# Optimization experiments

Hardware: AMD Instinct MI355X
Metric: run time of the kernel (lower is better)

Reference implementation:

```python
import jax, jax.numpy as jnp
import numpy as np
import math

B, N, D = 8, 4096, 1024
H = 8          # num_heads
NC = 2         # n_classes


def setup_inputs() -> dict:
    key = jax.random.key(0)
    ks = jax.random.split(key, 12)
    s = 1.0 / math.sqrt(D)
    return {
        "inputs": jax.random.normal(ks[0], (B, N, D), jnp.float32),
        # enc: Linear(D, 1) + Sigmoid
        "W_enc": jax.random.normal(ks[1], (1, D), jnp.float32) * s,
        "b_enc": jnp.zeros((1,), jnp.float32),
        "cls_token": jax.random.normal(ks[2], (1, 1, D), jnp.float32) * s,
        # depthwise Conv2d(D, D, 3, padding=1, groups=D)
        "conv_w": jax.random.normal(ks[3], (D, 1, 3, 3), jnp.float32) * 0.1,
        "conv_b": jnp.zeros((D,), jnp.float32),
        # MAB projections (torch Linear weight layout [out, in])
        "Wq": jax.random.normal(ks[4], (D, D), jnp.float32) * s,
        "bq": jnp.zeros((D,), jnp.float32),
        "Wk": jax.random.normal(ks[5], (D, D), jnp.float32) * s,
        "bk": jnp.zeros((D,), jnp.float32),
        "Wv": jax.random.normal(ks[6], (D, D), jnp.float32) * s,
        "bv": jnp.zeros((D,), jnp.float32),
        "Wo": jax.random.normal(ks[7], (D, D), jnp.float32) * s,
        "bo": jnp.zeros((D,), jnp.float32),
        # final classifier Linear(D, NC)
        "Wfc": jax.random.normal(ks[8], (NC, D), jnp.float32) * s,
        "bfc": jnp.zeros((NC,), jnp.float32),
    }


def reference(inputs, W_enc, b_enc, cls_token, conv_w, conv_b,
              Wq, bq, Wk, bk, Wv, bv, Wo, bo, Wfc, bfc):
    b, n, d = inputs.shape
    # ---- recalib(option='max', k=1): top-1 instance per bag as query ----
    a1 = jax.nn.sigmoid(inputs @ W_enc.T + b_enc)[..., 0]            # [B, N]
    idx = jnp.argmax(a1, axis=1)                                      # [B]
    Q = jnp.take_along_axis(inputs, idx[:, None, None], axis=1)       # [B, 1, D]
    # ---- shift_feature ----
    inputs = jax.nn.relu(inputs - Q)
    # ---- pad to square grid, prepend cls token ----
    _H = int(np.ceil(np.sqrt(n)))
    add = _H * _H - n
    x = jnp.concatenate([inputs, inputs[:, :add, :]], axis=1)         # [B, _H*_H, D]
    cls = jnp.broadcast_to(cls_token, (b, 1, d))
    x = jnp.concatenate([cls, x], axis=1)                             # [B, S, D]
    cls_tok, feat = x[:, 0], x[:, 1:]
    # ---- depthwise conv residual on the 2D grid ----
    cnn = feat.transpose(0, 2, 1).reshape(b, d, _H, _H)               # [B, C, H, W]
    conv = jax.lax.conv_general_dilated(
        cnn, conv_w, window_strides=(1, 1), padding='SAME',
        dimension_numbers=('NCHW', 'OIHW', 'NCHW'),
        feature_group_count=d) + conv_b[None, :, None, None]
    cnn = conv + cnn
    xf = cnn.reshape(b, d, _H * _H).transpose(0, 2, 1)
    x = jnp.concatenate([cls_tok[:, None, :], xf], axis=1)            # [B, S, D]
    # ---- MAB(Q, x): manual multi-head attention ----
    Qp = Q @ Wq.T + bq                                                # [B, 1, D]
    K = x @ Wk.T + bk                                                 # [B, S, D]
    V = x @ Wv.T + bv
    dh = d // H
    qh = Qp.reshape(b, 1, H, dh).transpose(0, 2, 1, 3)                # [B, H, 1, dh]
    kh = K.reshape(b, -1, H, dh).transpose(0, 2, 1, 3)                # [B, H, S, dh]
    vh = V.reshape(b, -1, H, dh).transpose(0, 2, 1, 3)
    # NOTE: original scales by sqrt(dim_V), not sqrt(d_head)
    logits = jnp.einsum('bhqd,bhkd->bhqk', qh, kh) / jnp.asarray(math.sqrt(d), jnp.float32)
    A = jax.nn.softmax(logits, axis=-1)
    oh = qh + jnp.einsum('bhqk,bhkd->bhqd', A, vh)                    # residual inside heads
    O = oh.transpose(0, 2, 1, 3).reshape(b, 1, d)                     # [B, 1, D]
    O = O + jax.nn.relu(O @ Wo.T + bo)
    bag = O[:, 0]                                                     # [B, D]
    out = bag @ Wfc.T + bfc                                           # [B, NC]
    return out
```

## Files before the change

### kernel.cpp

```cpp
#include <hip/hip_runtime.h>
#include <hip/hip_bf16.h>


#define NTOK 4096
#define DD 1024

#define FO_ARG 0
#define FO_S1  16
#define FO_CWT 4160
#define FO_QP  13376
#define FO_W   21568
#define FO_MS  87232
#define FO_YP  95424
#define FO_Y   4289728
#define FO_O1  4355264
#define FO_O2  4363456
#define FO_AW  4371648

#define LSTRIDE 101

__global__ void k_init(const float* __restrict__ convw, float* __restrict__ cwT) {
  int gid = blockIdx.x * 256 + threadIdx.x;
  if (gid < 9216) {
    int d = gid / 9, p = gid - d * 9;
    cwT[p * DD + d] = convw[gid];
  }
}

__global__ void k_argmax1(const float* __restrict__ inp, const float* __restrict__ Wenc,
                          const float* __restrict__ benc, unsigned long long* __restrict__ s1buf) {
  __shared__ unsigned long long lb[4];
  int wave = threadIdx.x >> 6, lane = threadIdx.x & 63;
  int b = blockIdx.x >> 8;
  int r0 = ((blockIdx.x & 255) << 4) + (wave << 2);
  const float4* base = (const float4*)(inp + ((size_t)b * NTOK + r0) * DD);
  const float4* wp = (const float4*)Wenc;
  float s0 = 0.f, s1 = 0.f, s2 = 0.f, s3 = 0.f;
#pragma unroll
  for (int k = 0; k < 4; ++k) {
    int off = lane + (k << 6);
    float4 w4 = wp[off];
    float4 a0 = base[off];
    float4 a1 = base[256 + off];
    float4 a2 = base[512 + off];
    float4 a3 = base[768 + off];
    s0 = fmaf(w4.x, a0.x, s0); s0 = fmaf(w4.y, a0.y, s0); s0 = fmaf(w4.z, a0.z, s0); s0 = fmaf(w4.w, a0.w, s0);
    s1 = fmaf(w4.x, a1.x, s1); s1 = fmaf(w4.y, a1.y, s1); s1 = fmaf(w4.z, a1.z, s1); s1 = fmaf(w4.w, a1.w, s1);
    s2 = fmaf(w4.x, a2.x, s2); s2 = fmaf(w4.y, a2.y, s2); s2 = fmaf(w4.z, a2.z, s2); s2 = fmaf(w4.w, a2.w, s2);
    s3 = fmaf(w4.x, a3.x, s3); s3 = fmaf(w4.y, a3.y, s3); s3 = fmaf(w4.z, a3.z, s3); s3 = fmaf(w4.w, a3.w, s3);
  }
#pragma unroll
  for (int mk = 32; mk >= 1; mk >>= 1) {
    s0 += __shfl_xor(s0, mk); s1 += __shfl_xor(s1, mk);
    s2 += __shfl_xor(s2, mk); s3 += __shfl_xor(s3, mk);
  }
  if (lane == 0) {
    float be = benc[0];
    float v[4] = {s0 + be, s1 + be, s2 + be, s3 + be};
    unsigned long long bst = 0ull;
#pragma unroll
    for (int i = 0; i < 4; ++i) {
      unsigned u = __float_as_uint(v[i]);
      u = (u & 0x80000000u) ? ~u : (u | 0x80000000u);
      unsigned long long p = ((unsigned long long)u << 32) |
                             (unsigned long long)(0xFFFFFFFFu - (unsigned)(r0 + i));
      bst = bst > p ? bst : p;
    }
    lb[wave] = bst;
  }
  __syncthreads();
  if (threadIdx.x == 0) {
    unsigned long long m = lb[0];
#pragma unroll
    for (int i = 1; i < 4; ++i) m = m > lb[i] ? m : lb[i];
    s1buf[blockIdx.x] = m;
  }
}

__global__ void k_argmax2(const unsigned long long* __restrict__ s1buf,
                          unsigned long long* __restrict__ argbest) {
  __shared__ unsigned long long red[256];
  int tid = threadIdx.x, b = blockIdx.x;
  red[tid] = s1buf[b * 256 + tid];
  __syncthreads();
  for (int s = 128; s > 0; s >>= 1) {
    if (tid < s) { unsigned long long o = red[tid + s]; if (o > red[tid]) red[tid] = o; }
    __syncthreads();
  }
  if (tid == 0) argbest[b] = red[0];
}

__global__ void k_qp(const float* __restrict__ inp, const float* __restrict__ Wq,
                     const float* __restrict__ bq, const unsigned long long* __restrict__ argbest,
                     float* __restrict__ Qp) {
  int wave = threadIdx.x >> 6, lane = threadIdx.x & 63;
  int b = blockIdx.x >> 8;
  int i = ((blockIdx.x & 255) << 2) + wave;
  unsigned idx = 0xFFFFFFFFu - (unsigned)(argbest[b] & 0xFFFFFFFFull);
  const float4* qr = (const float4*)(inp + ((size_t)b * NTOK + idx) * DD);
  const float4* wr = (const float4*)(Wq + (size_t)i * DD);
  float s = 0.f;
#pragma unroll
  for (int k = 0; k < 4; ++k) {
    float4 a = wr[lane + (k << 6)], x = qr[lane + (k << 6)];
    s = fmaf(a.x, x.x, s); s = fmaf(a.y, x.y, s);
    s = fmaf(a.z, x.z, s); s = fmaf(a.w, x.w, s);
  }
  for (int m = 32; m > 0; m >>= 1) s += __shfl_xor(s, m);
  if (lane == 0) Qp[b * DD + i] = s + bq[i];
}

__global__ void k_w(const float* __restrict__ Wk, const float* __restrict__ Qp,
                    float* __restrict__ wbuf) {
  __shared__ float qs[1024];
  __shared__ float sred[2048];
  const int tid = threadIdx.x;
  const int h = blockIdx.x >> 5, jb = blockIdx.x & 31;
  {
    int b = tid >> 5, i4 = tid & 31;
    ((float4*)qs)[b * 32 + i4] = ((const float4*)Qp)[b * 256 + (h << 5) + i4];
  }
  __syncthreads();
  const int jl = tid & 31, ig = tid >> 5;
  const float* wkp = Wk + (size_t)((h << 7) + (ig << 4)) * DD + (jb << 5) + jl;
  float acc[8];
#pragma unroll
  for (int b = 0; b < 8; ++b) acc[b] = 0.f;
#pragma unroll
  for (int ii = 0; ii < 16; ++ii) {
    float wv = wkp[(size_t)ii * DD];
    int i = (ig << 4) + ii;
#pragma unroll
    for (int b = 0; b < 8; ++b) acc[b] = fmaf(qs[(b << 7) + i], wv, acc[b]);
  }
#pragma unroll
  for (int b = 0; b < 8; ++b) sred[ig * 256 + (b << 5) + jl] = acc[b];
  __syncthreads();
  {
    int b = tid >> 5, j2 = tid & 31;
    float s = 0.f;
#pragma unroll
    for (int g = 0; g < 8; ++g) s += sred[g * 256 + (b << 5) + j2];
    wbuf[(size_t)((b << 3) + h) * DD + (jb << 5) + j2] = s;
  }
}

__global__ __launch_bounds__(512, 4) void k_logits(
    const float* __restrict__ inp, const float* __restrict__ convb,
    const float* __restrict__ cwT, const float* __restrict__ wbuf,
    const unsigned long long* __restrict__ argbest,
    float* __restrict__ plog) {
  __shared__ float4 sred4[32 * LSTRIDE];
  const int tid = threadIdx.x, bx = blockIdx.x;
  const int b = bx >> 9, tile = (bx >> 3) & 63, cidx = bx & 7;
  const int R0 = (tile >> 3) << 3, C0 = (tile & 7) << 3;
  const unsigned idxq = 0xFFFFFFFFu - (unsigned)(argbest[b] & 0xFFFFFFFFull);
  const float* inpb = inp + (size_t)b * NTOK * DD;
  const float* qrow = inpb + (size_t)idxq * DD;
  const int gg = tid & 31, ts = tid >> 5;
  const int jg = tid >> 5, rq = (tid >> 3) & 3, ca = tid & 7;
  const int r0a = rq << 1;
  const int jc = cidx << 7;

  float acc[2][8];
#pragma unroll
  for (int i = 0; i < 2; ++i)
#pragma unroll
    for (int h = 0; h < 8; ++h) acc[i][h] = 0.f;

  {
    const int js = jc + (gg << 2);
    float4 qv = *(const float4*)(qrow + js);
    for (int t = ts; t < 100; t += 16) {
      int tr = t / 10, tc = t - tr * 10;
      int gr = R0 - 1 + tr, gc = C0 - 1 + tc;
      float4 v = make_float4(0.f, 0.f, 0.f, 0.f);
      if (gr >= 0 && gr < 64 && gc >= 0 && gc < 64) {
        float4 rv = *(const float4*)(inpb + (size_t)((gr << 6) + gc) * DD + js);
        v.x = fmaxf(rv.x - qv.x, 0.f); v.y = fmaxf(rv.y - qv.y, 0.f);
        v.z = fmaxf(rv.z - qv.z, 0.f); v.w = fmaxf(rv.w - qv.w, 0.f);
      }
      sred4[gg * LSTRIDE + t] = v;
    }
  }
  __syncthreads();
#pragma unroll
  for (int sub = 0; sub < 2; ++sub) {
    const int g = (sub << 4) + jg;
    const int j4 = jc + (g << 2);
    float4 cwr[9];
#pragma unroll
    for (int p = 0; p < 9; ++p) cwr[p] = *(const float4*)(cwT + p * DD + j4);
    float4 cb4 = *(const float4*)(convb + j4);
    const float4* fb = sred4 + g * LSTRIDE;
    float4 x0 = cb4, x1 = cb4;
    {
      float4 rw[4][3];
#pragma unroll
      for (int rr = 0; rr < 4; ++rr)
#pragma unroll
        for (int dc = 0; dc < 3; ++dc)
          rw[rr][dc] = fb[(r0a + rr) * 10 + ca + dc];
#pragma unroll
      for (int dr = 0; dr < 3; ++dr)
#pragma unroll
        for (int dc = 0; dc < 3; ++dc) {
          float4 w = cwr[dr * 3 + dc];
          float4 f0 = rw[dr][dc], f1 = rw[dr + 1][dc];
          x0.x = fmaf(w.x, f0.x, x0.x); x0.y = fmaf(w.y, f0.y, x0.y);
          x0.z = fmaf(w.z, f0.z, x0.z); x0.w = fmaf(w.w, f0.w, x0.w);
          x1.x = fmaf(w.x, f1.x, x1.x); x1.y = fmaf(w.y, f1.y, x1.y);
          x1.z = fmaf(w.z, f1.z, x1.z); x1.w = fmaf(w.w, f1.w, x1.w);
        }
      x0.x += rw[1][1].x; x0.y += rw[1][1].y; x0.z += rw[1][1].z; x0.w += rw[1][1].w;
      x1.x += rw[2][1].x; x1.y += rw[2][1].y; x1.z += rw[2][1].z; x1.w += rw[2][1].w;
    }
#pragma unroll
    for (int h = 0; h < 8; ++h) {
      float4 whv = *(const float4*)(wbuf + (size_t)(b * 8 + h) * DD + j4);
      float a0 = acc[0][h], a1 = acc[1][h];
      a0 = fmaf(whv.x, x0.x, a0); a0 = fmaf(whv.y, x0.y, a0);
      a0 = fmaf(whv.z, x0.z, a0); a0 = fmaf(whv.w, x0.w, a0);
      a1 = fmaf(whv.x, x1.x, a1); a1 = fmaf(whv.y, x1.y, a1);
      a1 = fmaf(whv.z, x1.z, a1); a1 = fmaf(whv.w, x1.w, a1);
      acc[0][h] = a0; acc[1][h] = a1;
    }
  }
  __syncthreads();
  float* red = (float*)sred4;
#pragma unroll
  for (int it = 0; it < 2; ++it)
#pragma unroll
    for (int h = 0; h < 8; ++h)
      red[jg * 512 + ((r0a + it) * 8 + ca) * 8 + h] = acc[it][h];
  __syncthreads();
  {
    float s = 0.f;
#pragma unroll
    for (int g = 0; g < 16; ++g) s += red[g * 512 + tid];
    plog[(size_t)bx * 512 + tid] = s;
  }
}

__global__ void k_sm(const float* __restrict__ plog, float* __restrict__ aw,
                     float2* __restrict__ msbuf) {
  __shared__ float atile[512];
  const int tid = threadIdx.x, bt = blockIdx.x;
  const float* pp = plog + (size_t)bt * 8 * 512;
  float s0 = 0.f, s1 = 0.f;
#pragma unroll
  for (int c = 0; c < 8; ++c) {
    s0 += pp[c * 512 + tid];
    s1 += pp[c * 512 + 256 + tid];
  }
  {
    int o = tid, h = o & 7, tok = o >> 3;
    atile[h * 64 + tok] = s0 * 0.03125f;
    o = tid + 256; h = o & 7; tok = o >> 3;
    atile[h * 64 + tok] = s1 * 0.03125f;
  }
  __syncthreads();
  const int hh = tid >> 5, sl = tid & 31;
  float l1 = atile[hh * 64 + sl], l2 = atile[hh * 64 + 32 + sl];
  float mx = fmaxf(l1, l2);
#pragma unroll
  for (int mk = 16; mk >= 1; mk >>= 1) mx = fmaxf(mx, __shfl_xor(mx, mk));
  float e1 = __expf(l1 - mx), e2 = __expf(l2 - mx);
  float Ssum = e1 + e2;
#pragma unroll
  for (int mk = 16; mk >= 1; mk >>= 1) Ssum += __shfl_xor(Ssum, mk);
  aw[(size_t)bt * 512 + hh * 64 + sl] = e1;
  aw[(size_t)bt * 512 + hh * 64 + 32 + sl] = e2;
  if (sl == 0) {
    int b = bt >> 6, tile = bt & 63;
    msbuf[((b << 3) + hh) * 64 + tile] = make_float2(mx, Ssum);
  }
}

__global__ __launch_bounds__(512, 4) void k_yacc(
    const float* __restrict__ inp, const float* __restrict__ convb,
    const float* __restrict__ cwT, const float* __restrict__ aw,
    const unsigned long long* __restrict__ argbest,
    float* __restrict__ ypart) {
  __shared__ float4 sred4[32 * LSTRIDE];
  __shared__ float atile[512];
  const int tid = threadIdx.x, bx = blockIdx.x;
  const int b = bx >> 9, tile = (bx >> 3) & 63, cidx = bx & 7;
  const int R0 = (tile >> 3) << 3, C0 = (tile & 7) << 3;
  const unsigned idxq = 0xFFFFFFFFu - (unsigned)(argbest[b] & 0xFFFFFFFFull);
  const float* inpb = inp + (size_t)b * NTOK * DD;
  const float* qrow = inpb + (size_t)idxq * DD;
  const int gg = tid & 31, ts = tid >> 5;
  const int jc = cidx << 7;

  atile[tid] = aw[(size_t)((b << 6) + tile) * 512 + tid];
  {
    const int js = jc + (gg << 2);
    float4 qv = *(const float4*)(qrow + js);
    for (int t = ts; t < 100; t += 16) {
      int tr = t / 10, tc = t - tr * 10;
      int gr = R0 - 1 + tr, gc = C0 - 1 + tc;
      float4 v = make_float4(0.f, 0.f, 0.f, 0.f);
      if (gr >= 0 && gr < 64 && gc >= 0 && gc < 64) {
        float4 rv = *(const float4*)(inpb + (size_t)((gr << 6) + gc) * DD + js);
        v.x = fmaxf(rv.x - qv.x, 0.f); v.y = fmaxf(rv.y - qv.y, 0.f);
        v.z = fmaxf(rv.z - qv.z, 0.f); v.w = fmaxf(rv.w - qv.w, 0.f);
      }
      sred4[gg * LSTRIDE + t] = v;
    }
  }
  __syncthreads();
  const int gB = tid >> 4, rh = (tid >> 3) & 1, cB = tid & 7;
  const int rbase = rh << 2;
  const int j4 = jc + (gB << 2);
  float4 cwr[9];
#pragma unroll
  for (int p = 0; p < 9; ++p) cwr[p] = *(const float4*)(cwT + p * DD + j4);
  float4 cb4 = *(const float4*)(convb + j4);
  const float4* fb = sred4 + gB * LSTRIDE;
  float4 y4[8];
#pragma unroll
  for (int h = 0; h < 8; ++h) y4[h] = make_float4(0.f, 0.f, 0.f, 0.f);
  float4 w0[3], w1[3], w2[3];
#pragma unroll
  for (int dc = 0; dc < 3; ++dc) {
    w0[dc] = fb[rbase * 10 + cB + dc];
    w1[dc] = fb[(rbase + 1) * 10 + cB + dc];
  }
#pragma unroll
  for (int k = 0; k < 4; ++k) {
#pragma unroll
    for (int dc = 0; dc < 3; ++dc) w2[dc] = fb[(rbase + k + 2) * 10 + cB + dc];
    float4 x4 = cb4;
#pragma unroll
    for (int dc = 0; dc < 3; ++dc) {
      float4 wa = cwr[dc], wb = cwr[3 + dc], wc = cwr[6 + dc];
      x4.x = fmaf(wa.x, w0[dc].x, x4.x); x4.y = fmaf(wa.y, w0[dc].y, x4.y);
      x4.z = fmaf(wa.z, w0[dc].z, x4.z); x4.w = fmaf(wa.w, w0[dc].w, x4.w);
      x4.x = fmaf(wb.x, w1[dc].x, x4.x); x4.y = fmaf(wb.y, w1[dc].y, x4.y);
      x4.z = fmaf(wb.z, w1[dc].z, x4.z); x4.w = fmaf(wb.w, w1[dc].w, x4.w);
      x4.x = fmaf(wc.x, w2[dc].x, x4.x); x4.y = fmaf(wc.y, w2[dc].y, x4.y);
      x4.z = fmaf(wc.z, w2[dc].z, x4.z); x4.w = fmaf(wc.w, w2[dc].w, x4.w);
    }
    x4.x += w1[1].x; x4.y += w1[1].y; x4.z += w1[1].z; x4.w += w1[1].w;
    int tok = ((rbase + k) << 3) + cB;
#pragma unroll
    for (int h = 0; h < 8; ++h) {
      float a = atile[h * 64 + tok];
      y4[h].x = fmaf(a, x4.x, y4[h].x); y4[h].y = fmaf(a, x4.y, y4[h].y);
      y4[h].z = fmaf(a, x4.z, y4[h].z); y4[h].w = fmaf(a, x4.w, y4[h].w);
    }
#pragma unroll
    for (int dc = 0; dc < 3; ++dc) { w0[dc] = w1[dc]; w1[dc] = w2[dc]; }
  }
#pragma unroll
  for (int h = 0; h < 8; ++h)
#pragma unroll
    for (int mk = 8; mk >= 1; mk >>= 1) {
      y4[h].x += __shfl_xor(y4[h].x, mk);
      y4[h].y += __shfl_xor(y4[h].y, mk);
      y4[h].z += __shfl_xor(y4[h].z, mk);
      y4[h].w += __shfl_xor(y4[h].w, mk);
    }
  if ((tid & 15) == 0) {
#pragma unroll
    for (int h = 0; h < 8; ++h)
      *(float4*)(ypart + ((size_t)(b * 8 + h) * 64 + tile) * DD + j4) = y4[h];
  }
}

__global__ void k_comb(const float2* __restrict__ msbuf, const float* __restrict__ wbuf,
                       const float* __restrict__ cls, const float* __restrict__ ypart,
                       float* __restrict__ ybuf) {
  __shared__ float redl[256];
  __shared__ float wgt[64];
  __shared__ float wclss;
  __shared__ float4 sacc[256];
  int tid = threadIdx.x;
  int bh = blockIdx.x >> 3, cs = blockIdx.x & 7;
  {
    float4 a = ((const float4*)(wbuf + (size_t)bh * DD))[tid];
    float4 c = ((const float4*)cls)[tid];
    redl[tid] = a.x * c.x + a.y * c.y + a.z * c.z + a.w * c.w;
  }
  __syncthreads();
  for (int s = 128; s > 0; s >>= 1) { if (tid < s) redl[tid] += redl[tid + s]; __syncthreads(); }
  float l0 = redl[0] * 0.03125f;
  if (tid < 64) {
    float2 ms = msbuf[bh * 64 + tid];
    float m = ms.x, S = ms.y;
    float M = m;
#pragma unroll
    for (int mk = 32; mk >= 1; mk >>= 1) M = fmaxf(M, __shfl_xor(M, mk));
    M = fmaxf(M, l0);
    float w = __expf(m - M);
    float z = S * w;
#pragma unroll
    for (int mk = 32; mk >= 1; mk >>= 1) z += __shfl_xor(z, mk);
    float ec = __expf(l0 - M);
    float Z = z + ec;
    wgt[tid] = w / Z;
    if (tid == 0) wclss = ec / Z;
  }
  __syncthreads();
  int ch4 = (cs << 5) + (tid & 31);
  int tg = tid >> 5;
  const float* yp = ypart + (size_t)bh * 64 * DD + (ch4 << 2);
  float4 acc = make_float4(0.f, 0.f, 0.f, 0.f);
#pragma unroll
  for (int tt = 0; tt < 8; ++tt) {
    int t = tg * 8 + tt;
    float w = wgt[t];
    float4 v = *(const float4*)(yp + (size_t)t * DD);
    acc.x = fmaf(w, v.x, acc.x); acc.y = fmaf(w, v.y, acc.y);
    acc.z = fmaf(w, v.z, acc.z); acc.w = fmaf(w, v.w, acc.w);
  }
  sacc[tg * 32 + (tid & 31)] = acc;
  __syncthreads();
  if (tid < 32) {
    int c4 = (cs << 5) + tid;
    float4 s = sacc[tid];
#pragma unroll
    for (int g = 1; g < 8; ++g) {
      float4 v = sacc[g * 32 + tid];
      s.x += v.x; s.y += v.y; s.z += v.z; s.w += v.w;
    }
    float wc = wclss;
    float4 cv = *(const float4*)(cls + (c4 << 2));
    s.x = fmaf(wc, cv.x, s.x); s.y = fmaf(wc, cv.y, s.y);
    s.z = fmaf(wc, cv.z, s.z); s.w = fmaf(wc, cv.w, s.w);
    *(float4*)(ybuf + (size_t)bh * DD + (c4 << 2)) = s;
  }
}

__global__ void k_o1(const float* __restrict__ Wv, const float* __restrict__ bv,
                     const float* __restrict__ Qp, const float* __restrict__ ybuf,
                     float* __restrict__ O1) {
  int wave = threadIdx.x >> 6, lane = threadIdx.x & 63;
  int b = blockIdx.x >> 8;
  int i = ((blockIdx.x & 255) << 2) + wave;
  int h = i >> 7;
  const float4* wr = (const float4*)(Wv + (size_t)i * DD);
  const float4* yr = (const float4*)(ybuf + (size_t)(b * 8 + h) * DD);
  float s = 0.f;
#pragma unroll
  for (int k = 0; k < 4; ++k) {
    float4 a = wr[lane + (k << 6)], x = yr[lane + (k << 6)];
    s = fmaf(a.x, x.x, s); s = fmaf(a.y, x.y, s);
    s = fmaf(a.z, x.z, s); s = fmaf(a.w, x.w, s);
  }
  for (int m = 32; m > 0; m >>= 1) s += __shfl_xor(s, m);
  if (lane == 0) O1[b * DD + i] = Qp[b * DD + i] + bv[i] + s;
}

__global__ void k_o2(const float* __restrict__ Wo, const float* __restrict__ bo,
                     const float* __restrict__ O1, float* __restrict__ O2) {
  int wave = threadIdx.x >> 6, lane = threadIdx.x & 63;
  int b = blockIdx.x >> 8;
  int i = ((blockIdx.x & 255) << 2) + wave;
  const float4* wr = (const float4*)(Wo + (size_t)i * DD);
  const float4* xr = (const float4*)(O1 + (size_t)b * DD);
  float s = 0.f;
#pragma unroll
  for (int k = 0; k < 4; ++k) {
    float4 a = wr[lane + (k << 6)], x = xr[lane + (k << 6)];
    s = fmaf(a.x, x.x, s); s = fmaf(a.y, x.y, s);
    s = fmaf(a.z, x.z, s); s = fmaf(a.w, x.w, s);
  }
  for (int m = 32; m > 0; m >>= 1) s += __shfl_xor(s, m);
  if (lane == 0) O2[b * DD + i] = O1[b * DD + i] + fmaxf(s + bo[i], 0.f);
}

__global__ void k_out(const float* __restrict__ Wfc, const float* __restrict__ bfc,
                      const float* __restrict__ O2, float* __restrict__ out) {
  int wave = threadIdx.x >> 6, lane = threadIdx.x & 63;
  for (int p = wave; p < 16; p += 4) {
    int b = p >> 1, cc = p & 1;
    const float4* o = (const float4*)(O2 + (size_t)b * DD);
    const float4* wr = (const float4*)(Wfc + (size_t)cc * DD);
    float s = 0.f;
#pragma unroll
    for (int k = 0; k < 4; ++k) {
      float4 a = o[lane + (k << 6)], x = wr[lane + (k << 6)];
      s = fmaf(a.x, x.x, s); s = fmaf(a.y, x.y, s);
      s = fmaf(a.z, x.z, s); s = fmaf(a.w, x.w, s);
    }
    for (int m = 32; m > 0; m >>= 1) s += __shfl_xor(s, m);
    if (lane == 0) out[p] = s + bfc[cc];
  }
}

extern "C" void kernel_launch(void* const* d_in, const int* in_sizes, int n_in,
                              void* d_out, int out_size, void* d_ws, size_t ws_size,
                              hipStream_t stream) {
  const float* inp   = (const float*)d_in[0];
  const float* Wenc  = (const float*)d_in[1];
  const float* benc  = (const float*)d_in[2];
  const float* cls   = (const float*)d_in[3];
  const float* convw = (const float*)d_in[4];
  const float* convb = (const float*)d_in[5];
  const float* Wq    = (const float*)d_in[6];
  const float* bq    = (const float*)d_in[7];
  const float* Wk    = (const float*)d_in[8];
  const float* bv    = (const float*)d_in[11];
  const float* Wv    = (const float*)d_in[10];
  const float* Wo    = (const float*)d_in[12];
  const float* bo    = (const float*)d_in[13];
  const float* Wfc   = (const float*)d_in[14];
  const float* bfc   = (const float*)d_in[15];
  float* out = (float*)d_out;
  float* W = (float*)d_ws;
  unsigned long long* argbest = (unsigned long long*)(W + FO_ARG);
  unsigned long long* s1buf   = (unsigned long long*)(W + FO_S1);
  float* cwT   = W + FO_CWT;
  float* Qp    = W + FO_QP;
  float* wbuf  = W + FO_W;
  float2* msbuf = (float2*)(W + FO_MS);
  float* ypart = W + FO_YP;
  float* plog  = W + FO_YP;
  float* aw    = W + FO_AW;
  float* ybuf  = W + FO_Y;
  float* O1    = W + FO_O1;
  float* O2    = W + FO_O2;

  hipLaunchKernelGGL(k_init,    dim3(36),   dim3(256), 0, stream, convw, cwT);
  hipLaunchKernelGGL(k_argmax1, dim3(2048), dim3(256), 0, stream, inp, Wenc, benc, s1buf);
  hipLaunchKernelGGL(k_argmax2, dim3(8),    dim3(256), 0, stream, s1buf, argbest);
  hipLaunchKernelGGL(k_qp,      dim3(2048), dim3(256), 0, stream, inp, Wq, bq, argbest, Qp);
  hipLaunchKernelGGL(k_w,       dim3(256),  dim3(256), 0, stream, Wk, Qp, wbuf);
  hipLaunchKernelGGL(k_logits,  dim3(4096), dim3(512), 0, stream, inp, convb, cwT, wbuf, argbest, plog);
  hipLaunchKernelGGL(k_sm,      dim3(512),  dim3(256), 0, stream, plog, aw, msbuf);
  hipLaunchKernelGGL(k_yacc,    dim3(4096), dim3(512), 0, stream, inp, convb, cwT, aw, argbest, ypart);
  hipLaunchKernelGGL(k_comb,    dim3(512),  dim3(256), 0, stream, msbuf, wbuf, cls, ypart, ybuf);
  hipLaunchKernelGGL(k_o1,      dim3(2048), dim3(256), 0, stream, Wv, bv, Qp, ybuf, O1);
  hipLaunchKernelGGL(k_o2,      dim3(2048), dim3(256), 0, stream, Wo, bo, O1, O2);
  hipLaunchKernelGGL(k_out,     dim3(1),    dim3(256), 0, stream, Wfc, bfc, O2, out);
}
```

Baseline: 387.0 us.

## Materialize conv output in logits pass instead of recomputing it for value sum

k_logits now also writes the shifted, depthwise-convolved features for each tile to a new workspace buffer, staging them through LDS so the global stores are coalesced. The old k_yacc kernel, which reloaded the inputs with halo and recomputed the 3x3 conv, is replaced by a lighter k_ysum. k_ysum streams the stored features and applies the softmax weights, which k_sm now writes in a token-major layout. This drops the second convolution pass in exchange for an extra full-size write and read of about 128MB, plus a larger workspace that must fit the new offset.

```diff
diff --git a/kernel.cpp b/kernel.cpp
--- a/kernel.cpp
+++ b/kernel.cpp
@@ -16,6 +16,7 @@
 #define FO_O1  4355264
 #define FO_O2  4363456
 #define FO_AW  4371648
+#define FO_XF  8388608
 
 #define LSTRIDE 101
 
@@ -149,7 +150,7 @@
     const float* __restrict__ inp, const float* __restrict__ convb,
     const float* __restrict__ cwT, const float* __restrict__ wbuf,
     const unsigned long long* __restrict__ argbest,
-    float* __restrict__ plog) {
+    float* __restrict__ plog, float* __restrict__ xf) {
   __shared__ float4 sred4[32 * LSTRIDE];
   const int tid = threadIdx.x, bx = blockIdx.x;
   const int b = bx >> 9, tile = (bx >> 3) & 63, cidx = bx & 7;
@@ -167,6 +168,7 @@
   for (int i = 0; i < 2; ++i)
 #pragma unroll
     for (int h = 0; h < 8; ++h) acc[i][h] = 0.f;
+  float4 xs0[2], xs1[2];
 
   {
     const int js = jc + (gg << 2);
@@ -215,6 +217,7 @@
       x0.x += rw[1][1].x; x0.y += rw[1][1].y; x0.z += rw[1][1].z; x0.w += rw[1][1].w;
       x1.x += rw[2][1].x; x1.y += rw[2][1].y; x1.z += rw[2][1].z; x1.w += rw[2][1].w;
     }
+    xs0[sub] = x0; xs1[sub] = x1;
 #pragma unroll
     for (int h = 0; h < 8; ++h) {
       float4 whv = *(const float4*)(wbuf + (size_t)(b * 8 + h) * DD + j4);
@@ -240,6 +243,28 @@
     for (int g = 0; g < 16; ++g) s += red[g * 512 + tid];
     plog[(size_t)bx * 512 + tid] = s;
   }
+  __syncthreads();
+  float4* ldsx = sred4;
+  {
+    const int tk0 = (r0a << 3) + ca;
+#pragma unroll
+    for (int sub = 0; sub < 2; ++sub) {
+      int q = (sub << 4) + jg;
+      ldsx[tk0 * 33 + q] = xs0[sub];
+      ldsx[(tk0 + 8) * 33 + q] = xs1[sub];
+    }
+  }
+  __syncthreads();
+  {
+    float* xfb = xf + (size_t)((b << 6) + tile) * (64 * DD) + jc;
+#pragma unroll
+    for (int it = 0; it < 4; ++it) {
+      int idx = (it << 9) + tid;
+      int tk = idx >> 5, q = idx & 31;
+      float4 v = ldsx[tk * 33 + q];
+      *(float4*)(xfb + (size_t)tk * DD + (q << 2)) = v;
+    }
+  }
 }
 
 __global__ void k_sm(const float* __restrict__ plog, float* __restrict__ aw,
@@ -269,104 +294,43 @@
   float Ssum = e1 + e2;
 #pragma unroll
   for (int mk = 16; mk >= 1; mk >>= 1) Ssum += __shfl_xor(Ssum, mk);
-  aw[(size_t)bt * 512 + hh * 64 + sl] = e1;
-  aw[(size_t)bt * 512 + hh * 64 + 32 + sl] = e2;
+  aw[(size_t)bt * 512 + sl * 8 + hh] = e1;
+  aw[(size_t)bt * 512 + (32 + sl) * 8 + hh] = e2;
   if (sl == 0) {
     int b = bt >> 6, tile = bt & 63;
     msbuf[((b << 3) + hh) * 64 + tile] = make_float2(mx, Ssum);
   }
 }
 
-__global__ __launch_bounds__(512, 4) void k_yacc(
-    const float* __restrict__ inp, const float* __restrict__ convb,
-    const float* __restrict__ cwT, const float* __restrict__ aw,
-    const unsigned long long* __restrict__ argbest,
+__global__ __launch_bounds__(512, 8) void k_ysum(
+    const float* __restrict__ xf, const float* __restrict__ aw,
     float* __restrict__ ypart) {
-  __shared__ float4 sred4[32 * LSTRIDE];
   __shared__ float atile[512];
-  const int tid = threadIdx.x, bx = blockIdx.x;
-  const int b = bx >> 9, tile = (bx >> 3) & 63, cidx = bx & 7;
-  const int R0 = (tile >> 3) << 3, C0 = (tile & 7) << 3;
-  const unsigned idxq = 0xFFFFFFFFu - (unsigned)(argbest[b] & 0xFFFFFFFFull);
-  const float* inpb = inp + (size_t)b * NTOK * DD;
-  const float* qrow = inpb + (size_t)idxq * DD;
-  const int gg = tid & 31, ts = tid >> 5;
-  const int jc = cidx << 7;
-
-  atile[tid] = aw[(size_t)((b << 6) + tile) * 512 + tid];
-  {
-    const int js = jc + (gg << 2);
-    float4 qv = *(const float4*)(qrow + js);
-    for (int t = ts; t < 100; t += 16) {
-      int tr = t / 10, tc = t - tr * 10;
-      int gr = R0 - 1 + tr, gc = C0 - 1 + tc;
-      float4 v = make_float4(0.f, 0.f, 0.f, 0.f);
-      if (gr >= 0 && gr < 64 && gc >= 0 && gc < 64) {
-        float4 rv = *(const float4*)(inpb + (size_t)((gr << 6) + gc) * DD + js);
-        v.x = fmaxf(rv.x - qv.x, 0.f); v.y = fmaxf(rv.y - qv.y, 0.f);
-        v.z = fmaxf(rv.z - qv.z, 0.f); v.w = fmaxf(rv.w - qv.w, 0.f);
-      }
-      sred4[gg * LSTRIDE + t] = v;
-    }
-  }
-  __syncthreads();
-  const int gB = tid >> 4, rh = (tid >> 3) & 1, cB = tid & 7;
-  const int rbase = rh << 2;
-  const int j4 = jc + (gB << 2);
-  float4 cwr[9];
-#pragma unroll
-  for (int p = 0; p < 9; ++p) cwr[p] = *(const float4*)(cwT + p * DD + j4);
-  float4 cb4 = *(const float4*)(convb + j4);
-  const float4* fb = sred4 + gB * LSTRIDE;
-  float4 y4[8];
-#pragma unroll
-  for (int h = 0; h < 8; ++h) y4[h] = make_float4(0.f, 0.f, 0.f, 0.f);
-  float4 w0[3], w1[3], w2[3];
-#pragma unroll
-  for (int dc = 0; dc < 3; ++dc) {
-    w0[dc] = fb[rbase * 10 + cB + dc];
-    w1[dc] = fb[(rbase + 1) * 10 + cB + dc];
-  }
-#pragma unroll
-  for (int k = 0; k < 4; ++k) {
-#pragma unroll
-    for (int dc = 0; dc < 3; ++dc) w2[dc] = fb[(rbase + k + 2) * 10 + cB + dc];
-    float4 x4 = cb4;
-#pragma unroll
-    for (int dc = 0; dc < 3; ++dc) {
-      float4 wa = cwr[dc], wb = cwr[3 + dc], wc = cwr[6 + dc];
-      x4.x = fmaf(wa.x, w0[dc].x, x4.x); x4.y = fmaf(wa.y, w0[dc].y, x4.y);
-      x4.z = fmaf(wa.z, w0[dc].z, x4.z); x4.w = fmaf(wa.w, w0[dc].w, x4.w);
-      x4.x = fmaf(wb.x, w1[dc].x, x4.x); x4.y = fmaf(wb.y, w1[dc].y, x4.y);
-      x4.z = fmaf(wb.z, w1[dc].z, x4.z); x4.w = fmaf(wb.w, w1[dc].w, x4.w);
-      x4.x = fmaf(wc.x, w2[dc].x, x4.x); x4.y = fmaf(wc.y, w2[dc].y, x4.y);
-      x4.z = fmaf(wc.z, w2[dc].z, x4.z); x4.w = fmaf(wc.w, w2[dc].w, x4.w);
-    }
-    x4.x += w1[1].x; x4.y += w1[1].y; x4.z += w1[1].z; x4.w += w1[1].w;
-    int tok = ((rbase + k) << 3) + cB;
-#pragma unroll
-    for (int h = 0; h < 8; ++h) {
-      float a = atile[h * 64 + tok];
-      y4[h].x = fmaf(a, x4.x, y4[h].x); y4[h].y = fmaf(a, x4.y, y4[h].y);
-      y4[h].z = fmaf(a, x4.z, y4[h].z); y4[h].w = fmaf(a, x4.w, y4[h].w);
-    }
-#pragma unroll
-    for (int dc = 0; dc < 3; ++dc) { w0[dc] = w1[dc]; w1[dc] = w2[dc]; }
-  }
+  const int tid = threadIdx.x, bt = blockIdx.x;
+  atile[tid] = aw[(size_t)bt * 512 + tid];
+  __syncthreads();
+  const float* xbase = xf + (size_t)bt * (64 * DD) + (tid << 1);
+  float2 acc[8];
+#pragma unroll
+  for (int h = 0; h < 8; ++h) acc[h] = make_float2(0.f, 0.f);
+#pragma unroll 4
+  for (int t = 0; t < 64; ++t) {
+    float2 v = *(const float2*)(xbase + (size_t)t * DD);
+    float4 aA = *(const float4*)&atile[t * 8];
+    float4 aB = *(const float4*)&atile[t * 8 + 4];
+    acc[0].x = fmaf(aA.x, v.x, acc[0].x); acc[0].y = fmaf(aA.x, v.y, acc[0].y);
+    acc[1].x = fmaf(aA.y, v.x, acc[1].x); acc[1].y = fmaf(aA.y, v.y, acc[1].y);
+    acc[2].x = fmaf(aA.z, v.x, acc[2].x); acc[2].y = fmaf(aA.z, v.y, acc[2].y);
+    acc[3].x = fmaf(aA.w, v.x, acc[3].x); acc[3].y = fmaf(aA.w, v.y, acc[3].y);
+    acc[4].x = fmaf(aB.x, v.x, acc[4].x); acc[4].y = fmaf(aB.x, v.y, acc[4].y);
+    acc[5].x = fmaf(aB.y, v.x, acc[5].x); acc[5].y = fmaf(aB.y, v.y, acc[5].y);
+    acc[6].x = fmaf(aB.z, v.x, acc[6].x); acc[6].y = fmaf(aB.z, v.y, acc[6].y);
+    acc[7].x = fmaf(aB.w, v.x, acc[7].x); acc[7].y = fmaf(aB.w, v.y, acc[7].y);
+  }
+  const int b = bt >> 6, tile = bt & 63;
 #pragma unroll
   for (int h = 0; h < 8; ++h)
-#pragma unroll
-    for (int mk = 8; mk >= 1; mk >>= 1) {
-      y4[h].x += __shfl_xor(y4[h].x, mk);
-      y4[h].y += __shfl_xor(y4[h].y, mk);
-      y4[h].z += __shfl_xor(y4[h].z, mk);
-      y4[h].w += __shfl_xor(y4[h].w, mk);
-    }
-  if ((tid & 15) == 0) {
-#pragma unroll
-    for (int h = 0; h < 8; ++h)
-      *(float4*)(ypart + ((size_t)(b * 8 + h) * 64 + tile) * DD + j4) = y4[h];
-  }
+    *(float2*)(ypart + ((size_t)((b * 8 + h) * 64 + tile)) * DD + (tid << 1)) = acc[h];
 }
 
 __global__ void k_comb(const float2* __restrict__ msbuf, const float* __restrict__ wbuf,
@@ -519,6 +483,7 @@
   float* ypart = W + FO_YP;
   float* plog  = W + FO_YP;
   float* aw    = W + FO_AW;
+  float* xf    = W + FO_XF;
   float* ybuf  = W + FO_Y;
   float* O1    = W + FO_O1;
   float* O2    = W + FO_O2;
@@ -528,9 +493,9 @@
   hipLaunchKernelGGL(k_argmax2, dim3(8),    dim3(256), 0, stream, s1buf, argbest);
   hipLaunchKernelGGL(k_qp,      dim3(2048), dim3(256), 0, stream, inp, Wq, bq, argbest, Qp);
   hipLaunchKernelGGL(k_w,       dim3(256),  dim3(256), 0, stream, Wk, Qp, wbuf);
-  hipLaunchKernelGGL(k_logits,  dim3(4096), dim3(512), 0, stream, inp, convb, cwT, wbuf, argbest, plog);
+  hipLaunchKernelGGL(k_logits,  dim3(4096), dim3(512), 0, stream, inp, convb, cwT, wbuf, argbest, plog, xf);
   hipLaunchKernelGGL(k_sm,      dim3(512),  dim3(256), 0, stream, plog, aw, msbuf);
-  hipLaunchKernelGGL(k_yacc,    dim3(4096), dim3(512), 0, stream, inp, convb, cwT, aw, argbest, ypart);
+  hipLaunchKernelGGL(k_ysum,    dim3(512),  dim3(512), 0, stream, xf, aw, ypart);
   hipLaunchKernelGGL(k_comb,    dim3(512),  dim3(256), 0, stream, msbuf, wbuf, cls, ypart, ybuf);
   hipLaunchKernelGGL(k_o1,      dim3(2048), dim3(256), 0, stream, Wv, bv, Qp, ybuf, O1);
   hipLaunchKernelGGL(k_o2,      dim3(2048), dim3(256), 0, stream, Wo, bo, O1, O2);
```

Measured after the change: 358.3 us. 7.4% less time.
